# Optimization experiments

Measured on AMD Instinct MI355X. Metric: run time of the kernel, lower is better.

Reference implementation:

```python
import jax, jax.numpy as jnp
import numpy as np

# ---- static config (severity=3 -> params (0.4, 1, 1)) ----
B, C, H, W = 64, 3, 224, 224
SIGMA = 0.4
MAX_DELTA = 1
ITERATIONS = 1
RADIUS = int(4.0 * SIGMA + 0.5)  # scipy/skimage default truncate=4.0 -> radius 2
_x = np.arange(-RADIUS, RADIUS + 1, dtype=np.float64)
_k = np.exp(-0.5 * (_x / SIGMA) ** 2)
KERNEL = jnp.asarray(_k / _k.sum(), dtype=jnp.float32)  # 5 taps

# swap coordinate order: y = H-1..1 (outer), x = W-1..1 (inner), repeated ITERATIONS times
_ys = np.arange(H - MAX_DELTA, MAX_DELTA - 1, -1, dtype=np.int32)
_xs = np.arange(W - MAX_DELTA, MAX_DELTA - 1, -1, dtype=np.int32)
YS = jnp.asarray(np.tile(np.repeat(_ys, _xs.size), ITERATIONS))  # [ITER*N]
XS = jnp.asarray(np.tile(np.tile(_xs, _ys.size), ITERATIONS))    # [ITER*N]
N_SWAPS = YS.shape[0]


def _gaussian_blur(img):
    """Separable Gaussian, mode='nearest' (edge pad), img [B,H,W,C] float."""
    p = jnp.pad(img, ((0, 0), (RADIUS, RADIUS), (0, 0), (0, 0)), mode='edge')
    img = sum(KERNEL[i] * p[:, i:i + H] for i in range(2 * RADIUS + 1))
    p = jnp.pad(img, ((0, 0), (0, 0), (RADIUS, RADIUS), (0, 0)), mode='edge')
    img = sum(KERNEL[i] * p[:, :, i:i + W] for i in range(2 * RADIUS + 1))
    return img


def _swap_single(img, d):
    """Sequential random pixel swaps. img [H,W,C]; d [N_SWAPS,2] in {-1,0,1}."""
    def body(im, t):
        y, x, dy, dx = t
        yp = jnp.clip(y + dy, 0, H - 1)
        xp = jnp.clip(x + dx, 0, W - 1)
        a = im[y, x]
        b = im[yp, xp]
        # set order matches original temp-swap (self-swap is identity)
        im = im.at[y, x].set(b).at[yp, xp].set(a)
        return im, None
    im, _ = jax.lax.scan(body, img, (YS, XS, d[:, 0], d[:, 1]))
    return im


def setup_inputs() -> dict:
    key = jax.random.key(0)
    k1, k2 = jax.random.split(key)
    x = jax.random.uniform(k1, (B, C, H, W), dtype=jnp.float32)
    deltas = jax.random.randint(k2, (B, N_SWAPS, 2), 0, 3, dtype=jnp.int32)
    return {"x": x, "deltas": deltas}


def reference(x, deltas):
    # tensor_to_numpy_uint8: clamp(x*255) then byte() (truncation)
    img = jnp.floor(jnp.clip(x * 255.0, 0.0, 255.0))        # [B,C,H,W], uint8 values
    img = jnp.transpose(img, (0, 2, 3, 1))                   # [B,H,W,C]
    # first blur + np.uint8 cast (truncation)
    img = jnp.floor(_gaussian_blur(img / 255.0) * 255.0)
    # sequential random pixel swaps, per image
    d = deltas - 1                                           # values in {-1,0,1}
    img = jax.vmap(_swap_single)(img, d)
    # second blur, clip, uint8 cast, then /255 back to float tensor
    img = _gaussian_blur(img / 255.0)
    img = jnp.floor(jnp.clip(img * 255.0, 0.0, 255.0)) / 255.0
    return jnp.transpose(img, (0, 3, 1, 2))                  # [B,C,H,W]
```

## Files before the change

kernel.cpp:

```cpp
#include <hip/hip_runtime.h>
#include <hip/hip_bf16.h>

#define KW0 0.91921792f
#define KW1 0.04038762f
#define KW2 3.42560e-6f

#define HH 224
#define WW 224
#define NSW 49729
#define LEAF_SLOT 676
#define LEAF_IMG 150748
#define P_STRIDE 50176

__global__ __launch_bounds__(256) void build_kernel(const int* __restrict__ deltas,
                                                    unsigned short* __restrict__ leafG) {
    const int j = blockIdx.x;
    const int b = blockIdx.y;
    const int U = j * 32;

    __shared__ __align__(16) unsigned short smA[32 * LEAF_SLOT];
    __shared__ unsigned pk[32 * 29];

    const int tid = threadIdx.x;
    const int u = U + tid;

    {
        const int2* Dbase = (const int2*)deltas + (size_t)b * NSW + (size_t)U * 223;
        for (int w = tid; w < 32 * 28; w += 256) {
            const int r = w / 28, k = w - r * 28;
            if (U + r < 223) {
                const int base = r * 223 + 8 * k;
                unsigned word = 0;
#pragma unroll
                for (int jj = 0; jj < 8; ++jj) {
                    const int i = 8 * k + jj;
                    unsigned idx = 5u;
                    if (i < 223) {
                        int2 d = Dbase[base + jj];
                        unsigned px = (unsigned)d.x, py = (unsigned)d.y;
                        if (U + r == 0) px = min(px, 1u);
                        if (i == 0) py = min(py, 1u);
                        idx = px * 4u + py;
                    }
                    word |= idx << (4 * jj);
                }
                pk[r * 29 + k] = word;
            }
        }
    }
    __syncthreads();

    if (tid < 32 && u < 223) {
        const int y = 223 - u;
        const unsigned b0r = (unsigned)(y - 1) << 8;
        const unsigned b1r = (unsigned)y << 8;
        const unsigned b2r = (unsigned)(y + 1) << 8;
        unsigned short* Lf = &smA[tid * LEAF_SLOT];
        const unsigned* pkr = &pk[tid * 29];

        unsigned w00 = b0r + 222, w01 = b0r + 223, w02 = b0r + 224;
        unsigned w10 = b1r + 222, w11 = b1r + 223, w12 = b1r + 224;
        unsigned w20 = b2r + 222, w21 = b2r + 223, w22 = b2r + 224;

        unsigned wA_ = pkr[0], wB_ = pkr[1], wC_ = pkr[2];

#define GB_STEP(KK, CA, CB, CC) {                                               \
            const int x_ = 223 - (ibase + (KK));                                \
            const unsigned wsel_ = (((KK) >> 3) == 0) ? wA_                     \
                                 : ((((KK) >> 3) == 1) ? wB_ : wC_);            \
            const unsigned idx_ = (wsel_ >> (4 * ((KK) & 7))) & 15u;            \
            const unsigned pr_ = idx_ >> 2, pc_ = idx_ & 3u;                    \
            const bool pc0_ = (pc_ == 0u), pc1_ = (pc_ == 1u);                  \
            const bool pr0_ = (pr_ == 0u), pr1_ = (pr_ == 1u);                  \
            const unsigned s0_ = pc0_ ? w0##CA : (pc1_ ? w0##CB : w0##CC);      \
            const unsigned s1_ = pc0_ ? w1##CA : (pc1_ ? w1##CB : w1##CC);      \
            const unsigned s2_ = pc0_ ? w2##CA : (pc1_ ? w2##CB : w2##CC);      \
            const unsigned v_ = pr0_ ? s0_ : (pr1_ ? s1_ : s2_);                \
            const unsigned c_ = w1##CB;                                         \
            w0##CA = idx_ == 0u  ? c_ : w0##CA;                                 \
            w0##CB = idx_ == 1u  ? c_ : w0##CB;                                 \
            w0##CC = idx_ == 2u  ? c_ : w0##CC;                                 \
            w1##CA = idx_ == 4u  ? c_ : w1##CA;                                 \
            w1##CC = idx_ == 6u  ? c_ : w1##CC;                                 \
            w2##CA = idx_ == 8u  ? c_ : w2##CA;                                 \
            w2##CB = idx_ == 9u  ? c_ : w2##CB;                                 \
            w2##CC = idx_ == 10u ? c_ : w2##CC;                                 \
            w1##CB = v_;                                                        \
            Lf[x_ + 1]   = (unsigned short)w0##CC;                              \
            Lf[x_ + 225] = (unsigned short)w1##CC;                              \
            Lf[x_ + 449] = (unsigned short)w2##CC;                              \
            w0##CC = b0r + (unsigned)(x_ - 2);                                  \
            w1##CC = b1r + (unsigned)(x_ - 2);                                  \
            w2##CC = b2r + (unsigned)(x_ - 2);                                  \
        }
#define GB_TRIPLE(K0) GB_STEP((K0), 0, 1, 2) GB_STEP((K0)+1, 2, 0, 1) GB_STEP((K0)+2, 1, 2, 0)
        for (int blk = 0; blk < 9; ++blk) {
            const int ibase = 24 * blk;
            const unsigned nA_ = pkr[min(3 * blk + 3, 27)];
            const unsigned nB_ = pkr[min(3 * blk + 4, 27)];
            const unsigned nC_ = pkr[min(3 * blk + 5, 27)];
            GB_TRIPLE(0)  GB_TRIPLE(3)  GB_TRIPLE(6)  GB_TRIPLE(9)
            GB_TRIPLE(12) GB_TRIPLE(15) GB_TRIPLE(18) GB_TRIPLE(21)
            wA_ = nA_; wB_ = nB_; wC_ = nC_;
        }
        {
            const int ibase = 216;
            GB_TRIPLE(0) GB_TRIPLE(3) GB_STEP(6, 0, 1, 2)
        }
        Lf[1] = (unsigned short)w01; Lf[225] = (unsigned short)w11; Lf[449] = (unsigned short)w21;
        Lf[0] = (unsigned short)w00; Lf[224] = (unsigned short)w10; Lf[448] = (unsigned short)w20;
#undef GB_TRIPLE
#undef GB_STEP
    }
    __syncthreads();

    const int nuT = min(32, 223 - U);
    uint2* dst = (uint2*)(leafG + (size_t)b * LEAF_IMG + (size_t)U * LEAF_SLOT);
    const uint2* srcp = (const uint2*)smA;
    for (int l = tid; l < nuT * (LEAF_SLOT / 4); l += 256) dst[l] = srcp[l];
}

__global__ __launch_bounds__(256) void blur1_kernel(const float* __restrict__ x,
                                                    unsigned char* __restrict__ img) {
    const int rb = blockIdx.x, c = blockIdx.y, b = blockIdx.z;
    const int y0 = rb * 8;
    __shared__ float A[12][WW];
    __shared__ float Bv[8][WW];
    const float* xp = x + ((size_t)(b * 3 + c)) * HH * WW;

    for (int l = threadIdx.x; l < 12 * 56; l += 256) {
        int r = l / 56, k4 = (l - r * 56) * 4;
        int gy = min(max(y0 + r - 2, 0), HH - 1);
        float4 v = *(const float4*)(xp + gy * WW + k4);
        A[r][k4]     = floorf(fminf(fmaxf(v.x * 255.0f, 0.0f), 255.0f));
        A[r][k4 + 1] = floorf(fminf(fmaxf(v.y * 255.0f, 0.0f), 255.0f));
        A[r][k4 + 2] = floorf(fminf(fmaxf(v.z * 255.0f, 0.0f), 255.0f));
        A[r][k4 + 3] = floorf(fminf(fmaxf(v.w * 255.0f, 0.0f), 255.0f));
    }
    __syncthreads();
    for (int l = threadIdx.x; l < 8 * WW; l += 256) {
        int r = l / WW, xx = l - r * WW;
        Bv[r][xx] = KW2 * A[r][xx] + KW1 * A[r + 1][xx] + KW0 * A[r + 2][xx]
                  + KW1 * A[r + 3][xx] + KW2 * A[r + 4][xx];
    }
    __syncthreads();
    unsigned char* op = img + ((size_t)(b * 3 + c)) * HH * WW;
    for (int l = threadIdx.x; l < 8 * WW; l += 256) {
        int r = l / WW, xx = l - r * WW;
        int c0 = max(xx - 2, 0), c1 = max(xx - 1, 0);
        int c3 = min(xx + 1, WW - 1), c4 = min(xx + 2, WW - 1);
        float s = KW2 * Bv[r][c0] + KW1 * Bv[r][c1] + KW0 * Bv[r][xx]
                + KW1 * Bv[r][c3] + KW2 * Bv[r][c4];
        op[(y0 + r) * WW + xx] = (unsigned char)floorf(s);
    }
}

__global__ __launch_bounds__(256) void chaseP_kernel(const unsigned short* __restrict__ leafG,
                                                     unsigned short* __restrict__ P) {
    const int b = blockIdx.y;
    const int base = blockIdx.x * 2048;
    const unsigned short* L = leafG + (size_t)b * LEAF_IMG;
    unsigned short* Pb = P + (size_t)b * P_STRIDE;
    const int e0 = base + (int)threadIdx.x * 8;
    if (e0 >= P_STRIDE) return;

    unsigned rv[8], cv[8]; bool done[8]; int us[8];
    const int pr0 = e0 / 224, pc0 = e0 - pr0 * 224;
    int umax = -1;
#pragma unroll
    for (int t = 0; t < 8; ++t) {
        const int pc = pc0 + t;
        const int pr = pr0 + (pc >= 224 ? 1 : 0);
        rv[t] = (unsigned)pr;
        cv[t] = (unsigned)(pc >= 224 ? pc - 224 : pc);
        us[t] = min(222, 224 - pr);
        done[t] = false;
        umax = max(umax, us[t]);
    }
    for (int u = umax; u >= 0; --u) {
        const unsigned short* Lu = L + u * LEAF_SLOT;
        const int bot = 222 - u;
        bool all = true;
#pragma unroll
        for (int t = 0; t < 8; ++t) {
            if (!done[t] && u <= us[t]) {
                if ((int)rv[t] < bot) done[t] = true;
                else {
                    const unsigned q = Lu[__mul24((int)rv[t] - bot, 224) + (int)cv[t]];
                    rv[t] = q >> 8;
                    cv[t] = q & 255u;
                }
            }
            all = all && done[t];
        }
        if (all) break;
    }
    unsigned res[8];
#pragma unroll
    for (int t = 0; t < 8; ++t)
        res[t] = (unsigned)(__mul24((int)rv[t], 224) + (int)cv[t]);
    uint4 v;
    v.x = res[0] | (res[1] << 16);
    v.y = res[2] | (res[3] << 16);
    v.z = res[4] | (res[5] << 16);
    v.w = res[6] | (res[7] << 16);
    *(uint4*)(Pb + e0) = v;
}

__global__ __launch_bounds__(256) void apply_kernel(unsigned char* __restrict__ img,
                                                    const unsigned short* __restrict__ P) {
    const int plane = blockIdx.x;
    const int b = plane / 3;
    __shared__ __align__(16) unsigned char im[HH * WW];
    unsigned char* g = img + (size_t)plane * (HH * WW);
    for (int l = threadIdx.x; l < (HH * WW) / 16; l += 256)
        ((int4*)im)[l] = ((const int4*)g)[l];
    __syncthreads();
    const unsigned short* Pp = P + (size_t)b * P_STRIDE;
    for (int t = threadIdx.x; t < (HH * WW) / 8; t += 256) {
        uint4 pe = ((const uint4*)Pp)[t];
        unsigned e0 = pe.x & 0xffffu, e1 = pe.x >> 16;
        unsigned e2 = pe.y & 0xffffu, e3 = pe.y >> 16;
        unsigned e4 = pe.z & 0xffffu, e5 = pe.z >> 16;
        unsigned e6 = pe.w & 0xffffu, e7 = pe.w >> 16;
        unsigned lo = (unsigned)im[e0] | ((unsigned)im[e1] << 8)
                    | ((unsigned)im[e2] << 16) | ((unsigned)im[e3] << 24);
        unsigned hi = (unsigned)im[e4] | ((unsigned)im[e5] << 8)
                    | ((unsigned)im[e6] << 16) | ((unsigned)im[e7] << 24);
        ((uint2*)g)[t] = make_uint2(lo, hi);
    }
}

__global__ __launch_bounds__(256) void blur2_kernel(const unsigned char* __restrict__ img,
                                                    float* __restrict__ out) {
    const int rb = blockIdx.x, c = blockIdx.y, b = blockIdx.z;
    const int y0 = rb * 8;
    __shared__ float A[12][WW];
    __shared__ float Bv[8][WW];
    const unsigned char* ip = img + ((size_t)(b * 3 + c)) * HH * WW;

    for (int l = threadIdx.x; l < 12 * WW; l += 256) {
        int r = l / WW, xx = l - r * WW;
        int gy = min(max(y0 + r - 2, 0), HH - 1);
        A[r][xx] = (float)ip[gy * WW + xx];
    }
    __syncthreads();
    for (int l = threadIdx.x; l < 8 * WW; l += 256) {
        int r = l / WW, xx = l - r * WW;
        Bv[r][xx] = KW2 * A[r][xx] + KW1 * A[r + 1][xx] + KW0 * A[r + 2][xx]
                  + KW1 * A[r + 3][xx] + KW2 * A[r + 4][xx];
    }
    __syncthreads();
    float* op = out + ((size_t)(b * 3 + c)) * HH * WW;
    for (int l = threadIdx.x; l < 8 * WW; l += 256) {
        int r = l / WW, xx = l - r * WW;
        int c0 = max(xx - 2, 0), c1 = max(xx - 1, 0);
        int c3 = min(xx + 1, WW - 1), c4 = min(xx + 2, WW - 1);
        float s = KW2 * Bv[r][c0] + KW1 * Bv[r][c1] + KW0 * Bv[r][xx]
                + KW1 * Bv[r][c3] + KW2 * Bv[r][c4];
        s = fminf(fmaxf(s, 0.0f), 255.0f);
        op[(y0 + r) * WW + xx] = floorf(s) / 255.0f;
    }
}

__global__ __launch_bounds__(256) void blur2_apply_kernel(const unsigned char* __restrict__ img,
                                                          const unsigned short* __restrict__ P,
                                                          float* __restrict__ out) {
    const int rb = blockIdx.x, c = blockIdx.y, b = blockIdx.z;
    const int y0 = rb * 8;
    __shared__ float A[12][WW];
    __shared__ float Bv[8][WW];
    const unsigned char* ip = img + ((size_t)(b * 3 + c)) * HH * WW;
    const unsigned short* Pp = P + (size_t)b * P_STRIDE;

    for (int l = threadIdx.x; l < 12 * WW; l += 256) {
        int r = l / WW, xx = l - r * WW;
        int gy = min(max(y0 + r - 2, 0), HH - 1);
        unsigned q = Pp[gy * WW + xx];
        A[r][xx] = (float)ip[q];
    }
    __syncthreads();
    for (int l = threadIdx.x; l < 8 * WW; l += 256) {
        int r = l / WW, xx = l - r * WW;
        Bv[r][xx] = KW2 * A[r][xx] + KW1 * A[r + 1][xx] + KW0 * A[r + 2][xx]
                  + KW1 * A[r + 3][xx] + KW2 * A[r + 4][xx];
    }
    __syncthreads();
    float* op = out + ((size_t)(b * 3 + c)) * HH * WW;
    for (int l = threadIdx.x; l < 8 * WW; l += 256) {
        int r = l / WW, xx = l - r * WW;
        int c0 = max(xx - 2, 0), c1 = max(xx - 1, 0);
        int c3 = min(xx + 1, WW - 1), c4 = min(xx + 2, WW - 1);
        float s = KW2 * Bv[r][c0] + KW1 * Bv[r][c1] + KW0 * Bv[r][xx]
                + KW1 * Bv[r][c3] + KW2 * Bv[r][c4];
        s = fminf(fmaxf(s, 0.0f), 255.0f);
        op[(y0 + r) * WW + xx] = floorf(s) / 255.0f;
    }
}

extern "C" void kernel_launch(void* const* d_in, const int* in_sizes, int n_in,
                              void* d_out, int out_size, void* d_ws, size_t ws_size,
                              hipStream_t stream) {
    const float* x      = (const float*)d_in[0];
    const int*   deltas = (const int*)d_in[1];
    float*       out    = (float*)d_out;
    unsigned char* img  = (unsigned char*)d_ws;

    unsigned short* leafG = (unsigned short*)d_out;
    unsigned short* pFall = leafG + (size_t)64 * LEAF_IMG;

    const bool fused = ws_size >= (size_t)9633792 + (size_t)64 * P_STRIDE * 2;
    unsigned short* P = fused ? (unsigned short*)(img + 9633792) : pFall;

    build_kernel<<<dim3(7, 64), 256, 0, stream>>>(deltas, leafG);
    blur1_kernel<<<dim3(28, 3, 64), 256, 0, stream>>>(x, img);
    chaseP_kernel<<<dim3(25, 64), 256, 0, stream>>>(leafG, P);

    dim3 gb(28, 3, 64);
    if (fused) {
        blur2_apply_kernel<<<gb, 256, 0, stream>>>(img, P, out);
    } else {
        apply_kernel<<<dim3(192), 256, 0, stream>>>(img, P);
        blur2_kernel<<<gb, 256, 0, stream>>>(img, out);
    }
}
```

Measured before the change: 120.5 us.

## Fuse permutation chase into second blur kernel, computing only needed window

Replaces the separate chaseP kernel (which writes a full per-image permutation P to global memory) and the blur2_apply kernel with one final_kernel. For each 8-row band plus halo, it chases the leaf tables itself, keeps the 12-row permutation window in shared memory, and reuses it for all three channels. The leaf tables move into the workspace instead of d_out when the workspace is large enough. This removes a launch and the P round trip, but chase work on the 4 halo rows is duplicated across neighbouring blocks, and the grid shrinks from 28x3x64 to 28x64 blocks, each looping serially over the three channels.

New measurement: 153.1 us. +27.1%, slower.

```diff
diff --git a/kernel.cpp b/kernel.cpp
--- a/kernel.cpp
+++ b/kernel.cpp
@@ -155,6 +155,87 @@
     }
 }
 
+__global__ __launch_bounds__(256) void final_kernel(const unsigned char* __restrict__ img,
+                                                    const unsigned short* __restrict__ leafG,
+                                                    float* __restrict__ out) {
+    const int rb = blockIdx.x, b = blockIdx.y;
+    const int y0 = rb * 8;
+    __shared__ unsigned short Pwin[12 * WW];
+    __shared__ float A[12][WW];
+    __shared__ float Bv[8][WW];
+    const unsigned short* L = leafG + (size_t)b * LEAF_IMG;
+    const int tid = threadIdx.x;
+
+    {
+        unsigned rv[11], cv[11]; bool done[11]; int us[11];
+        int umax = -1;
+#pragma unroll
+        for (int t = 0; t < 11; ++t) {
+            const int e = tid + t * 256;
+            const bool has = e < 12 * WW;
+            const int ec = has ? e : 0;
+            const int rr = ec / WW, xx = ec - (ec / WW) * WW;
+            const int gy = min(max(y0 + rr - 2, 0), HH - 1);
+            rv[t] = (unsigned)gy;
+            cv[t] = (unsigned)xx;
+            us[t] = has ? min(222, 224 - gy) : -1;
+            done[t] = !has;
+            if (has) umax = max(umax, us[t]);
+        }
+        for (int u = umax; u >= 0; --u) {
+            const unsigned short* Lu = L + u * LEAF_SLOT;
+            const int bot = 222 - u;
+            bool all = true;
+#pragma unroll
+            for (int t = 0; t < 11; ++t) {
+                if (!done[t] && u <= us[t]) {
+                    if ((int)rv[t] < bot) done[t] = true;
+                    else {
+                        const unsigned q = Lu[__mul24((int)rv[t] - bot, 224) + (int)cv[t]];
+                        rv[t] = q >> 8;
+                        cv[t] = q & 255u;
+                    }
+                }
+                all = all && done[t];
+            }
+            if (all) break;
+        }
+#pragma unroll
+        for (int t = 0; t < 11; ++t) {
+            const int e = tid + t * 256;
+            if (e < 12 * WW)
+                Pwin[e] = (unsigned short)(__mul24((int)rv[t], 224) + (int)cv[t]);
+        }
+    }
+    __syncthreads();
+
+    for (int c = 0; c < 3; ++c) {
+        const unsigned char* ip = img + ((size_t)(b * 3 + c)) * HH * WW;
+        for (int l = tid; l < 12 * WW; l += 256) {
+            int r = l / WW, xx = l - (l / WW) * WW;
+            A[r][xx] = (float)ip[Pwin[l]];
+        }
+        __syncthreads();
+        for (int l = tid; l < 8 * WW; l += 256) {
+            int r = l / WW, xx = l - (l / WW) * WW;
+            Bv[r][xx] = KW2 * A[r][xx] + KW1 * A[r + 1][xx] + KW0 * A[r + 2][xx]
+                      + KW1 * A[r + 3][xx] + KW2 * A[r + 4][xx];
+        }
+        __syncthreads();
+        float* op = out + ((size_t)(b * 3 + c)) * HH * WW;
+        for (int l = tid; l < 8 * WW; l += 256) {
+            int r = l / WW, xx = l - (l / WW) * WW;
+            int c0 = max(xx - 2, 0), c1 = max(xx - 1, 0);
+            int c3 = min(xx + 1, WW - 1), c4 = min(xx + 2, WW - 1);
+            float s = KW2 * Bv[r][c0] + KW1 * Bv[r][c1] + KW0 * Bv[r][xx]
+                    + KW1 * Bv[r][c3] + KW2 * Bv[r][c4];
+            s = fminf(fmaxf(s, 0.0f), 255.0f);
+            op[(y0 + r) * WW + xx] = floorf(s) / 255.0f;
+        }
+        __syncthreads();
+    }
+}
+
 __global__ __launch_bounds__(256) void chaseP_kernel(const unsigned short* __restrict__ leafG,
                                                      unsigned short* __restrict__ P) {
     const int b = blockIdx.y;
@@ -263,41 +344,6 @@
     }
 }
 
-__global__ __launch_bounds__(256) void blur2_apply_kernel(const unsigned char* __restrict__ img,
-                                                          const unsigned short* __restrict__ P,
-                                                          float* __restrict__ out) {
-    const int rb = blockIdx.x, c = blockIdx.y, b = blockIdx.z;
-    const int y0 = rb * 8;
-    __shared__ float A[12][WW];
-    __shared__ float Bv[8][WW];
-    const unsigned char* ip = img + ((size_t)(b * 3 + c)) * HH * WW;
-    const unsigned short* Pp = P + (size_t)b * P_STRIDE;
-
-    for (int l = threadIdx.x; l < 12 * WW; l += 256) {
-        int r = l / WW, xx = l - r * WW;
-        int gy = min(max(y0 + r - 2, 0), HH - 1);
-        unsigned q = Pp[gy * WW + xx];
-        A[r][xx] = (float)ip[q];
-    }
-    __syncthreads();
-    for (int l = threadIdx.x; l < 8 * WW; l += 256) {
-        int r = l / WW, xx = l - r * WW;
-        Bv[r][xx] = KW2 * A[r][xx] + KW1 * A[r + 1][xx] + KW0 * A[r + 2][xx]
-                  + KW1 * A[r + 3][xx] + KW2 * A[r + 4][xx];
-    }
-    __syncthreads();
-    float* op = out + ((size_t)(b * 3 + c)) * HH * WW;
-    for (int l = threadIdx.x; l < 8 * WW; l += 256) {
-        int r = l / WW, xx = l - r * WW;
-        int c0 = max(xx - 2, 0), c1 = max(xx - 1, 0);
-        int c3 = min(xx + 1, WW - 1), c4 = min(xx + 2, WW - 1);
-        float s = KW2 * Bv[r][c0] + KW1 * Bv[r][c1] + KW0 * Bv[r][xx]
-                + KW1 * Bv[r][c3] + KW2 * Bv[r][c4];
-        s = fminf(fmaxf(s, 0.0f), 255.0f);
-        op[(y0 + r) * WW + xx] = floorf(s) / 255.0f;
-    }
-}
-
 extern "C" void kernel_launch(void* const* d_in, const int* in_sizes, int n_in,
                               void* d_out, int out_size, void* d_ws, size_t ws_size,
                               hipStream_t stream) {
@@ -306,21 +352,22 @@
     float*       out    = (float*)d_out;
     unsigned char* img  = (unsigned char*)d_ws;
 
-    unsigned short* leafG = (unsigned short*)d_out;
-    unsigned short* pFall = leafG + (size_t)64 * LEAF_IMG;
-
-    const bool fused = ws_size >= (size_t)9633792 + (size_t)64 * P_STRIDE * 2;
-    unsigned short* P = fused ? (unsigned short*)(img + 9633792) : pFall;
-
-    build_kernel<<<dim3(7, 64), 256, 0, stream>>>(deltas, leafG);
-    blur1_kernel<<<dim3(28, 3, 64), 256, 0, stream>>>(x, img);
-    chaseP_kernel<<<dim3(25, 64), 256, 0, stream>>>(leafG, P);
-
-    dim3 gb(28, 3, 64);
-    if (fused) {
-        blur2_apply_kernel<<<gb, 256, 0, stream>>>(img, P, out);
+    const size_t imgBytes  = 9633792;
+    const size_t leafBytes = (size_t)64 * LEAF_IMG * 2;
+    const bool big_ws = ws_size >= imgBytes + leafBytes;
+
+    if (big_ws) {
+        unsigned short* leafG = (unsigned short*)(img + imgBytes);
+        build_kernel<<<dim3(7, 64), 256, 0, stream>>>(deltas, leafG);
+        blur1_kernel<<<dim3(28, 3, 64), 256, 0, stream>>>(x, img);
+        final_kernel<<<dim3(28, 64), 256, 0, stream>>>(img, leafG, out);
     } else {
-        apply_kernel<<<dim3(192), 256, 0, stream>>>(img, P);
-        blur2_kernel<<<gb, 256, 0, stream>>>(img, out);
-    }
-}
+        unsigned short* leafG = (unsigned short*)d_out;
+        unsigned short* pF    = leafG + (size_t)64 * LEAF_IMG;
+        build_kernel<<<dim3(7, 64), 256, 0, stream>>>(deltas, leafG);
+        blur1_kernel<<<dim3(28, 3, 64), 256, 0, stream>>>(x, img);
+        chaseP_kernel<<<dim3(25, 64), 256, 0, stream>>>(leafG, pF);
+        apply_kernel<<<dim3(192), 256, 0, stream>>>(img, pF);
+        blur2_kernel<<<dim3(28, 3, 64), 256, 0, stream>>>(img, out);
+    }
+}
```
